# Kernel tuning notes

Measured on AMD Instinct MI355X. Metric: run time of the kernel, lower is better.

Reference implementation:

```python
import jax, jax.numpy as jnp
import numpy as np

B, C, H, W = 4, 512, 64, 64
MID = C // 8  # 64


def setup_inputs() -> dict:
    key = jax.random.key(0)
    ks = jax.random.split(key, 8)
    s = 0.02
    return {
        "x": jax.random.normal(ks[0], (B, C, H, W), dtype=jnp.float32),
        "Wq": jax.random.normal(ks[1], (MID, C), dtype=jnp.float32) * s,
        "bq": jax.random.normal(ks[2], (MID,), dtype=jnp.float32) * s,
        "Wk": jax.random.normal(ks[3], (MID, C), dtype=jnp.float32) * s,
        "bk": jax.random.normal(ks[4], (MID,), dtype=jnp.float32) * s,
        "Wv": jax.random.normal(ks[5], (C, C), dtype=jnp.float32) * s,
        "bv": jax.random.normal(ks[6], (C,), dtype=jnp.float32) * s,
        "gamma": jax.random.uniform(ks[7], (1,), dtype=jnp.float32),
    }


def reference(x, Wq, bq, Wk, bk, Wv, bv, gamma):
    b, c, h, w = x.shape
    n = h * w
    xf = x.reshape(b, c, n)  # [B, C, N]
    # 1x1 convs are per-position linear maps
    q = jnp.einsum('mc,bcn->bnm', Wq, xf) + bq            # [B, N, mid]
    k = jnp.einsum('mc,bcn->bmn', Wk, xf) + bk[:, None]   # [B, mid, N]
    sim = jax.nn.softmax(jnp.einsum('bnm,bmj->bnj', q, k), axis=-1)  # [B, N, N]
    v = jnp.einsum('dc,bcn->bdn', Wv, xf) + bv[:, None]   # [B, C, N]
    # feat[:, d, i] = sum_j v[:, d, j] * sim[:, i, j]
    feat = jnp.einsum('bdj,bij->bdi', v, sim)             # [B, C, N]
    out = gamma[0] * feat + xf
    return out.reshape(b, c, h, w)
```

## Files before the change

### kernel.cpp

```cpp
#include <hip/hip_runtime.h>

#define BATCH 4
#define CCH   512
#define NN    4096
#define MIDD  64

typedef unsigned short u16;
typedef unsigned int   u32;
typedef short s8v  __attribute__((ext_vector_type(8)));
typedef float f16v __attribute__((ext_vector_type(16)));

__device__ __forceinline__ u16 f2bf(float f) {
  u32 u = __float_as_uint(f);
  u += 0x7fffu + ((u >> 16) & 1u);
  return (u16)(u >> 16);
}

__device__ __forceinline__ void g2lds16(const u16* g, u16* l) {
  __builtin_amdgcn_global_load_lds(
      (const __attribute__((address_space(1))) u32*)(const void*)g,
      (__attribute__((address_space(3))) u32*)(void*)l, 16, 0, 0);
}

#define S_WAITCNT(vm, lgkm) \
  __builtin_amdgcn_s_waitcnt(((vm) & 15) | (((vm) >> 4) << 14) | (0x7 << 4) | ((lgkm) << 8))

__global__ __launch_bounds__(256) void prep_w(
    const float* __restrict__ Wq, const float* __restrict__ Wk,
    const float* __restrict__ Wv, u16* __restrict__ Wb)
{
  int e = (blockIdx.x * 256 + threadIdx.x) * 8;
  const float* src;
  if (e < 64 * 512)       src = Wq + e;
  else if (e < 128 * 512) src = Wk + (e - 64 * 512);
  else                    src = Wv + (e - 128 * 512);
  float4 v0 = *(const float4*)src;
  float4 v1 = *(const float4*)(src + 4);
  uint4 p;
  p.x = (u32)f2bf(v0.x) | ((u32)f2bf(v0.y) << 16);
  p.y = (u32)f2bf(v0.z) | ((u32)f2bf(v0.w) << 16);
  p.z = (u32)f2bf(v1.x) | ((u32)f2bf(v1.y) << 16);
  p.w = (u32)f2bf(v1.z) | ((u32)f2bf(v1.w) << 16);
  *(uint4*)(Wb + e) = p;
}

__global__ __launch_bounds__(256) void transpose_cast(
    const float* __restrict__ x, u16* __restrict__ xbT)
{
  const int b  = blockIdx.z;
  const int c0 = blockIdx.y * 64;
  const int n0 = blockIdx.x * 64;
  const int t  = threadIdx.x;
  __shared__ float ts[64 * 65];

  #pragma unroll
  for (int k = 0; k < 4; k++) {
    int idx = t + 256 * k;
    int cc = idx >> 4, n4 = idx & 15;
    float4 v = *(const float4*)&x[((size_t)(b * CCH + c0 + cc)) * NN + n0 + n4 * 4];
    float* p = &ts[cc * 65 + n4 * 4];
    p[0] = v.x; p[1] = v.y; p[2] = v.z; p[3] = v.w;
  }
  __syncthreads();

  const int n = t >> 2, cb = (t & 3) * 16;
  u16 tmp[16];
  #pragma unroll
  for (int j = 0; j < 16; j++) tmp[j] = f2bf(ts[(cb + j) * 65 + n]);
  u16* dst = &xbT[((size_t)b * NN + n0 + n) * CCH + c0 + cb];
  *(uint4*)&dst[0] = *(uint4*)&tmp[0];
  *(uint4*)&dst[8] = *(uint4*)&tmp[8];
}

__global__ __launch_bounds__(256, 2) void proj_gemm(
    const u16* __restrict__ xbT, const u16* __restrict__ Wb,
    const float* __restrict__ bq, const float* __restrict__ bk,
    const float* __restrict__ bv,
    u16* __restrict__ qT, u16* __restrict__ kT, u16* __restrict__ vT)
{
  const int b  = blockIdx.z;
  const int mt = blockIdx.y;
  const int n0 = blockIdx.x * 256;
  const int t  = threadIdx.x;
  const int ln = t & 31, hi = (t & 63) >> 5, w = t >> 6;
  const int l  = t & 63;
  const int l2 = l & 3, lr = l >> 2;
  const int swc = (l2 ^ (lr & 3)) * 8;

  const int mrow0 = (mt < 8) ? (128 + mt * 64) : ((mt == 8) ? 0 : 64);
  const float* bias = (mt < 8) ? (bv + mt * 64) : ((mt == 8) ? bq : bk);

  __shared__ u16 ws[2][64 * 32];
  __shared__ u16 xs[2][256 * 32];

  const u16* xsrc = xbT + ((size_t)b * NN + n0 + w * 64 + lr) * CCH + swc;
  const u16* wsrc = Wb + (size_t)(mrow0 + w * 16 + lr) * 512 + swc;

  f16v acc[4];
  #pragma unroll
  for (int i = 0; i < 4; i++)
    #pragma unroll
    for (int r = 0; r < 16; r++) acc[i][r] = 0.f;

  #pragma unroll
  for (int i = 0; i < 4; i++)
    g2lds16(xsrc + (size_t)(16 * i) * CCH, &xs[0][(w * 64 + i * 16) * 32]);
  g2lds16(wsrc, &ws[0][w * 16 * 32]);

  for (int it = 0; it < 16; it++) {
    const int cur = it & 1, nxt = cur ^ 1;
    __builtin_amdgcn_s_barrier();
    const int c1 = ((it + 1) & 15) * 32;
    #pragma unroll
    for (int i = 0; i < 4; i++)
      g2lds16(xsrc + (size_t)(16 * i) * CCH + c1, &xs[nxt][(w * 64 + i * 16) * 32]);
    g2lds16(wsrc + c1, &ws[nxt][w * 16 * 32]);

    S_WAITCNT(5, 15);
    __builtin_amdgcn_s_barrier();

    #pragma unroll
    for (int ks = 0; ks < 2; ks++) {
      const int cb = ((2 * ks + hi) ^ (ln & 3)) << 3;
      s8v a0 = *(const s8v*)&ws[cur][(ln)           * 32 + cb];
      s8v a1 = *(const s8v*)&ws[cur][(32 + ln)      * 32 + cb];
      s8v b0 = *(const s8v*)&xs[cur][(w * 64 + ln)      * 32 + cb];
      s8v b1 = *(const s8v*)&xs[cur][(w * 64 + 32 + ln) * 32 + cb];
      acc[0] = __builtin_amdgcn_mfma_f32_32x32x16_bf16(a0, b0, acc[0], 0, 0, 0);
      acc[1] = __builtin_amdgcn_mfma_f32_32x32x16_bf16(a0, b1, acc[1], 0, 0, 0);
      acc[2] = __builtin_amdgcn_mfma_f32_32x32x16_bf16(a1, b0, acc[2], 0, 0, 0);
      acc[3] = __builtin_amdgcn_mfma_f32_32x32x16_bf16(a1, b1, acc[3], 0, 0, 0);
    }
  }

  S_WAITCNT(0, 0);
  __builtin_amdgcn_s_barrier();

  if (mt < 8) {
    const int m0g = mt * 64;
    #pragma unroll
    for (int mi = 0; mi < 2; mi++)
      #pragma unroll
      for (int ni = 0; ni < 2; ni++) {
        f16v& a = acc[mi * 2 + ni];
        #pragma unroll
        for (int r = 0; r < 16; r++) {
          int row = (r & 3) + 8 * (r >> 2) + 4 * hi;
          int m   = mi * 32 + row;
          float val = a[r] + bias[m];
          vT[((size_t)b * CCH + m0g + m) * NN + n0 + w * 64 + ni * 32 + ln] = f2bf(val);
        }
      }
  } else {
    u16* dst = (mt == 8) ? qT : kT;
    u16* xt  = &xs[0][0];
    #pragma unroll
    for (int mi = 0; mi < 2; mi++)
      #pragma unroll
      for (int ni = 0; ni < 2; ni++) {
        f16v& a = acc[mi * 2 + ni];
        #pragma unroll
        for (int r = 0; r < 16; r++) {
          int row = (r & 3) + 8 * (r >> 2) + 4 * hi;
          int m   = mi * 32 + row;
          int nr  = w * 64 + ni * 32 + ln;
          xt[(nr << 6) + (((m >> 3) ^ (ln & 7)) << 3) + (m & 7)] = f2bf(a[r] + bias[m]);
        }
      }
    __syncthreads();
    const int r7 = t & 7;
    u16* drow = &dst[((size_t)b * NN + n0 + t) * 64];
    #pragma unroll
    for (int k = 0; k < 8; k++)
      *(uint4*)&drow[k * 8] = *(uint4*)&xt[(t << 6) + ((k ^ r7) << 3)];
  }
}

__global__ __launch_bounds__(256, 2) void attn_kernel(
    const u16* __restrict__ qT,
    const u16* __restrict__ kT,
    const u16* __restrict__ vT,
    const float* __restrict__ x,
    const float* __restrict__ gamma,
    float* __restrict__ out)
{
  __shared__ u16 ksm[2][64 * 64];
  __shared__ u16 plm[2][64 * 64];
  __shared__ u16 vsm[256 * 64];

  const int bx    = blockIdx.x;
  const int slot  = bx & 7;
  const int b     = slot >> 1;
  const int dbase = (slot & 1) * 256;
  const int i0    = (bx >> 3) * 64;
  const int t     = threadIdx.x;
  const int l     = t & 63, ln = l & 31, hi = l >> 5;
  const int w     = t >> 6;
  const int qh    = w >> 1;
  const int jh    = w & 1;
  const int l3    = l & 7, lh3 = l >> 3;
  const int sw8   = (l3 ^ lh3) * 8;

  s8v qfrag[4];
  {
    const u16* qp = qT + ((size_t)b * NN + i0 + qh * 32 + ln) * 64 + hi * 8;
    #pragma unroll
    for (int k = 0; k < 4; k++) qfrag[k] = *(const s8v*)(qp + 16 * k);
  }

  const u16* kbase = kT + (size_t)b * NN * 64;
  const u16* vbase = vT + ((size_t)b * CCH + dbase) * NN;
  const u16* ksrc  = kbase + (size_t)(16 * w + lh3) * 64 + sw8;
  const u16* vsrc  = vbase + (size_t)(64 * w + lh3) * NN + sw8;

  f16v oacc[4];
  #pragma unroll
  for (int i = 0; i < 4; i++)
    #pragma unroll
    for (int r = 0; r < 16; r++) oacc[i][r] = 0.f;
  float lpart[16];
  #pragma unroll
  for (int r = 0; r < 16; r++) lpart[r] = 0.f;

  #pragma unroll
  for (int i = 0; i < 2; i++)
    g2lds16(ksrc + (size_t)(8 * i) * 64, &ksm[0][(w * 2 + i) * 512]);

  for (int it = 0; it < 64; it++) {
    const int j0  = it * 64;
    const int cur = it & 1, nxt = cur ^ 1;

    __builtin_amdgcn_s_barrier();
    #pragma unroll
    for (int i = 0; i < 8; i++)
      g2lds16(vsrc + (size_t)(8 * i) * NN + j0, vsm + (w * 8 + i) * 512);
    const int j1 = ((it + 1) & 63) * 64;
    #pragma unroll
    for (int i = 0; i < 2; i++)
      g2lds16(ksrc + (size_t)(j1 + 8 * i) * 64, &ksm[nxt][(w * 2 + i) * 512]);

    S_WAITCNT(10, 15);
    __builtin_amdgcn_s_barrier();

    f16v sacc;
    #pragma unroll
    for (int r = 0; r < 16; r++) sacc[r] = 0.f;
    #pragma unroll
    for (int ks = 0; ks < 4; ks++) {
      s8v bf = *(const s8v*)&ksm[cur][(jh * 32 + ln) * 64 + (((2 * ks + hi) ^ l3) << 3)];
      sacc = __builtin_amdgcn_mfma_f32_32x32x16_bf16(qfrag[ks], bf, sacc, 0, 0, 0);
    }
    #pragma unroll
    for (int r = 0; r < 16; r++) {
      float p = __expf(sacc[r]);
      lpart[r] += p;
      int row = qh * 32 + (r & 3) + ((r >> 2) << 3) + (hi << 2);
      int r7  = (r & 3) + (hi << 2);
      int jbl = (jh << 2) + (ln >> 3);
      plm[cur][(row << 6) + ((jbl ^ r7) << 3) + (ln & 7)] = f2bf(p);
    }

    S_WAITCNT(2, 0);
    __builtin_amdgcn_s_barrier();

    #pragma unroll
    for (int ks = 0; ks < 4; ks++) {
      const int cb = ((2 * ks + hi) ^ l3) << 3;
      s8v p0 = *(const s8v*)&plm[cur][(ln << 6) + cb];
      s8v p1 = *(const s8v*)&plm[cur][((32 + ln) << 6) + cb];
      s8v v0 = *(const s8v*)&vsm[(((w << 5) + ln) << 6) + cb];
      s8v v1 = *(const s8v*)&vsm[((((w + 4) << 5) + ln) << 6) + cb];
      oacc[0] = __builtin_amdgcn_mfma_f32_32x32x16_bf16(v0, p0, oacc[0], 0, 0, 0);
      oacc[1] = __builtin_amdgcn_mfma_f32_32x32x16_bf16(v0, p1, oacc[1], 0, 0, 0);
      oacc[2] = __builtin_amdgcn_mfma_f32_32x32x16_bf16(v1, p0, oacc[2], 0, 0, 0);
      oacc[3] = __builtin_amdgcn_mfma_f32_32x32x16_bf16(v1, p1, oacc[3], 0, 0, 0);
    }
  }

  S_WAITCNT(0, 0);
  __builtin_amdgcn_s_barrier();

  float* lred = (float*)&ksm[0][0];
  #pragma unroll
  for (int r = 0; r < 16; r++) {
    float v = lpart[r];
    v += __shfl_xor(v, 1);  v += __shfl_xor(v, 2);  v += __shfl_xor(v, 4);
    v += __shfl_xor(v, 8);  v += __shfl_xor(v, 16);
    lpart[r] = v;
  }
  if (ln == 0) {
    #pragma unroll
    for (int r = 0; r < 16; r++) {
      int row = qh * 32 + (r & 3) + ((r >> 2) << 3) + (hi << 2);
      lred[jh * 64 + row] = lpart[r];
    }
  }
  __syncthreads();

  const float g0 = gamma[0];
  #pragma unroll
  for (int qt = 0; qt < 2; qt++) {
    const float linv = 1.0f / (lred[qt * 32 + ln] + lred[64 + qt * 32 + ln]);
    const int n = i0 + qt * 32 + ln;
    #pragma unroll
    for (int ds = 0; ds < 2; ds++) {
      f16v& a = oacc[ds * 2 + qt];
      const int dg = dbase + (w + 4 * ds) * 32;
      #pragma unroll
      for (int r = 0; r < 16; r++) {
        int dl = (r & 3) + 8 * (r >> 2) + 4 * hi;
        size_t idx = ((size_t)b * CCH + dg + dl) * NN + n;
        out[idx] = g0 * a[r] * linv + x[idx];
      }
    }
  }
}

extern "C" void kernel_launch(void* const* d_in, const int* in_sizes, int n_in,
                              void* d_out, int out_size, void* d_ws, size_t ws_size,
                              hipStream_t stream) {
  const float* x     = (const float*)d_in[0];
  const float* Wq    = (const float*)d_in[1];
  const float* bq    = (const float*)d_in[2];
  const float* Wk    = (const float*)d_in[3];
  const float* bk    = (const float*)d_in[4];
  const float* Wv    = (const float*)d_in[5];
  const float* bv    = (const float*)d_in[6];
  const float* gamma = (const float*)d_in[7];
  float* out = (float*)d_out;

  u16* qT  = (u16*)d_ws;
  u16* kT  = qT  + (size_t)BATCH * NN * MIDD;
  u16* vT  = kT  + (size_t)BATCH * NN * MIDD;
  u16* xbT = vT  + (size_t)BATCH * CCH * NN;
  u16* Wb  = xbT + (size_t)BATCH * NN * CCH;

  prep_w<<<dim3(160), 256, 0, stream>>>(Wq, Wk, Wv, Wb);
  transpose_cast<<<dim3(NN / 64, CCH / 64, BATCH), 256, 0, stream>>>(x, xbT);
  proj_gemm<<<dim3(NN / 256, 10, BATCH), 256, 0, stream>>>(
      xbT, Wb, bq, bk, bv, qT, kT, vT);
  attn_kernel<<<dim3(512), 256, 0, stream>>>(qT, kT, vT, x, gamma, out);
}
```

Before: 234.1 us.

## Fuse x transpose/cast into projection GEMM and retile to 128x128 blocks

Removes the separate transpose_cast kernel and its bf16 transposed copy of x. The projection GEMM now loads fp32 x tiles directly into LDS, converts and transposes them in shared memory, and computes 128-row output groups, with q and k merged into one group. Biases are packed into a single buffer by prep_w. This saves a full write and read of a 16 MB intermediate and one launch, but the GEMM loop loses its double buffering, adds extra barriers, and re-reads x five times in fp32.

```diff
diff --git a/kernel.cpp b/kernel.cpp
--- a/kernel.cpp
+++ b/kernel.cpp
@@ -16,10 +16,10 @@
   return (u16)(u >> 16);
 }
 
-__device__ __forceinline__ void g2lds16(const u16* g, u16* l) {
+__device__ __forceinline__ void g2lds16(const void* g, void* l) {
   __builtin_amdgcn_global_load_lds(
-      (const __attribute__((address_space(1))) u32*)(const void*)g,
-      (__attribute__((address_space(3))) u32*)(void*)l, 16, 0, 0);
+      (const __attribute__((address_space(1))) u32*)g,
+      (__attribute__((address_space(3))) u32*)l, 16, 0, 0);
 }
 
 #define S_WAITCNT(vm, lgkm) \
@@ -27,74 +27,53 @@
 
 __global__ __launch_bounds__(256) void prep_w(
     const float* __restrict__ Wq, const float* __restrict__ Wk,
-    const float* __restrict__ Wv, u16* __restrict__ Wb)
-{
-  int e = (blockIdx.x * 256 + threadIdx.x) * 8;
-  const float* src;
-  if (e < 64 * 512)       src = Wq + e;
-  else if (e < 128 * 512) src = Wk + (e - 64 * 512);
-  else                    src = Wv + (e - 128 * 512);
-  float4 v0 = *(const float4*)src;
-  float4 v1 = *(const float4*)(src + 4);
-  uint4 p;
-  p.x = (u32)f2bf(v0.x) | ((u32)f2bf(v0.y) << 16);
-  p.y = (u32)f2bf(v0.z) | ((u32)f2bf(v0.w) << 16);
-  p.z = (u32)f2bf(v1.x) | ((u32)f2bf(v1.y) << 16);
-  p.w = (u32)f2bf(v1.z) | ((u32)f2bf(v1.w) << 16);
-  *(uint4*)(Wb + e) = p;
-}
-
-__global__ __launch_bounds__(256) void transpose_cast(
-    const float* __restrict__ x, u16* __restrict__ xbT)
-{
-  const int b  = blockIdx.z;
-  const int c0 = blockIdx.y * 64;
-  const int n0 = blockIdx.x * 64;
-  const int t  = threadIdx.x;
-  __shared__ float ts[64 * 65];
-
-  #pragma unroll
-  for (int k = 0; k < 4; k++) {
-    int idx = t + 256 * k;
-    int cc = idx >> 4, n4 = idx & 15;
-    float4 v = *(const float4*)&x[((size_t)(b * CCH + c0 + cc)) * NN + n0 + n4 * 4];
-    float* p = &ts[cc * 65 + n4 * 4];
-    p[0] = v.x; p[1] = v.y; p[2] = v.z; p[3] = v.w;
-  }
-  __syncthreads();
-
-  const int n = t >> 2, cb = (t & 3) * 16;
-  u16 tmp[16];
-  #pragma unroll
-  for (int j = 0; j < 16; j++) tmp[j] = f2bf(ts[(cb + j) * 65 + n]);
-  u16* dst = &xbT[((size_t)b * NN + n0 + n) * CCH + c0 + cb];
-  *(uint4*)&dst[0] = *(uint4*)&tmp[0];
-  *(uint4*)&dst[8] = *(uint4*)&tmp[8];
-}
-
-__global__ __launch_bounds__(256, 2) void proj_gemm(
-    const u16* __restrict__ xbT, const u16* __restrict__ Wb,
+    const float* __restrict__ Wv,
     const float* __restrict__ bq, const float* __restrict__ bk,
     const float* __restrict__ bv,
+    u16* __restrict__ Wb, float* __restrict__ bb)
+{
+  const int bid = blockIdx.x;
+  const int t   = threadIdx.x;
+  if (bid < 160) {
+    int e = (bid * 256 + t) * 8;
+    const float* src;
+    if (e < 64 * 512)       src = Wq + e;
+    else if (e < 128 * 512) src = Wk + (e - 64 * 512);
+    else                    src = Wv + (e - 128 * 512);
+    float4 v0 = *(const float4*)src;
+    float4 v1 = *(const float4*)(src + 4);
+    uint4 p;
+    p.x = (u32)f2bf(v0.x) | ((u32)f2bf(v0.y) << 16);
+    p.y = (u32)f2bf(v0.z) | ((u32)f2bf(v0.w) << 16);
+    p.z = (u32)f2bf(v1.x) | ((u32)f2bf(v1.y) << 16);
+    p.w = (u32)f2bf(v1.z) | ((u32)f2bf(v1.w) << 16);
+    *(uint4*)(Wb + e) = p;
+  } else if (t < 160) {
+    int e = t * 4;
+    const float* s = (t < 16) ? (bq + e) : (t < 32) ? (bk + (e - 64)) : (bv + (e - 128));
+    *(float4*)&bb[e] = *(const float4*)s;
+  }
+}
+
+__global__ __launch_bounds__(256, 2) void proj_gemm(
+    const float* __restrict__ x, const u16* __restrict__ Wb,
+    const float* __restrict__ bb,
     u16* __restrict__ qT, u16* __restrict__ kT, u16* __restrict__ vT)
 {
-  const int b  = blockIdx.z;
-  const int mt = blockIdx.y;
-  const int n0 = blockIdx.x * 256;
+  __shared__ char smem[32768];
+  float* xf  = (float*)smem;
+  u16*   xb  = (u16*)(smem + 16384);
+  u16*   wsm = (u16*)(smem + 24576);
+
+  const int b     = blockIdx.z;
+  const int g     = blockIdx.y;
+  const int gn0   = blockIdx.x * 128;
+  const int mrow0 = g * 128;
   const int t  = threadIdx.x;
-  const int ln = t & 31, hi = (t & 63) >> 5, w = t >> 6;
-  const int l  = t & 63;
-  const int l2 = l & 3, lr = l >> 2;
-  const int swc = (l2 ^ (lr & 3)) * 8;
-
-  const int mrow0 = (mt < 8) ? (128 + mt * 64) : ((mt == 8) ? 0 : 64);
-  const float* bias = (mt < 8) ? (bv + mt * 64) : ((mt == 8) ? bq : bk);
-
-  __shared__ u16 ws[2][64 * 32];
-  __shared__ u16 xs[2][256 * 32];
-
-  const u16* xsrc = xbT + ((size_t)b * NN + n0 + w * 64 + lr) * CCH + swc;
-  const u16* wsrc = Wb + (size_t)(mrow0 + w * 16 + lr) * 512 + swc;
+  const int l  = t & 63, ln = l & 31, hi = l >> 5, w = t >> 6;
+
+  const float* xsrc = x + ((size_t)(b * CCH) + w * 8 + (l >> 5)) * NN + gn0 + (l & 31) * 4;
+  const u16* wsrc = Wb + (size_t)(mrow0 + w * 32 + (l >> 2)) * 512 + ((l & 3) ^ ((l >> 2) & 3)) * 8;
 
   f16v acc[4];
   #pragma unroll
@@ -102,77 +81,78 @@
     #pragma unroll
     for (int r = 0; r < 16; r++) acc[i][r] = 0.f;
 
-  #pragma unroll
-  for (int i = 0; i < 4; i++)
-    g2lds16(xsrc + (size_t)(16 * i) * CCH, &xs[0][(w * 64 + i * 16) * 32]);
-  g2lds16(wsrc, &ws[0][w * 16 * 32]);
+  const int nrow = t >> 1, ch = (t & 1) * 16;
 
   for (int it = 0; it < 16; it++) {
-    const int cur = it & 1, nxt = cur ^ 1;
-    __builtin_amdgcn_s_barrier();
-    const int c1 = ((it + 1) & 15) * 32;
+    const int c0 = it * 32;
+    __syncthreads();
     #pragma unroll
     for (int i = 0; i < 4; i++)
-      g2lds16(xsrc + (size_t)(16 * i) * CCH + c1, &xs[nxt][(w * 64 + i * 16) * 32]);
-    g2lds16(wsrc + c1, &ws[nxt][w * 16 * 32]);
-
-    S_WAITCNT(5, 15);
-    __builtin_amdgcn_s_barrier();
+      g2lds16(xsrc + (size_t)(c0 + 2 * i) * NN, xf + (w * 8 + 2 * i) * 128);
+    #pragma unroll
+    for (int i = 0; i < 2; i++)
+      g2lds16(wsrc + (size_t)(i * 16) * 512 + c0, wsm + (w * 32 + i * 16) * 32);
+    __syncthreads();
+
+    u32 pk[8];
+    #pragma unroll
+    for (int j2 = 0; j2 < 8; j2++) {
+      float f0 = xf[(ch + 2 * j2 + 0) * 128 + nrow];
+      float f1 = xf[(ch + 2 * j2 + 1) * 128 + nrow];
+      pk[j2] = (u32)f2bf(f0) | ((u32)f2bf(f1) << 16);
+    }
+    #pragma unroll
+    for (int p2 = 0; p2 < 2; p2++) {
+      int phys = ((ch >> 3) + p2) ^ (nrow & 3);
+      *(uint4*)&xb[(nrow << 5) + (phys << 3)] =
+          make_uint4(pk[p2 * 4], pk[p2 * 4 + 1], pk[p2 * 4 + 2], pk[p2 * 4 + 3]);
+    }
+    __syncthreads();
 
     #pragma unroll
     for (int ks = 0; ks < 2; ks++) {
       const int cb = ((2 * ks + hi) ^ (ln & 3)) << 3;
-      s8v a0 = *(const s8v*)&ws[cur][(ln)           * 32 + cb];
-      s8v a1 = *(const s8v*)&ws[cur][(32 + ln)      * 32 + cb];
-      s8v b0 = *(const s8v*)&xs[cur][(w * 64 + ln)      * 32 + cb];
-      s8v b1 = *(const s8v*)&xs[cur][(w * 64 + 32 + ln) * 32 + cb];
-      acc[0] = __builtin_amdgcn_mfma_f32_32x32x16_bf16(a0, b0, acc[0], 0, 0, 0);
-      acc[1] = __builtin_amdgcn_mfma_f32_32x32x16_bf16(a0, b1, acc[1], 0, 0, 0);
-      acc[2] = __builtin_amdgcn_mfma_f32_32x32x16_bf16(a1, b0, acc[2], 0, 0, 0);
-      acc[3] = __builtin_amdgcn_mfma_f32_32x32x16_bf16(a1, b1, acc[3], 0, 0, 0);
-    }
-  }
-
-  S_WAITCNT(0, 0);
-  __builtin_amdgcn_s_barrier();
-
-  if (mt < 8) {
-    const int m0g = mt * 64;
-    #pragma unroll
-    for (int mi = 0; mi < 2; mi++)
+      s8v bf = *(const s8v*)&xb[((w * 32 + ln) << 5) + cb];
       #pragma unroll
-      for (int ni = 0; ni < 2; ni++) {
-        f16v& a = acc[mi * 2 + ni];
-        #pragma unroll
-        for (int r = 0; r < 16; r++) {
-          int row = (r & 3) + 8 * (r >> 2) + 4 * hi;
-          int m   = mi * 32 + row;
-          float val = a[r] + bias[m];
-          vT[((size_t)b * CCH + m0g + m) * NN + n0 + w * 64 + ni * 32 + ln] = f2bf(val);
-        }
+      for (int ms = 0; ms < 4; ms++) {
+        s8v af = *(const s8v*)&wsm[((ms * 32 + ln) << 5) + cb];
+        acc[ms] = __builtin_amdgcn_mfma_f32_32x32x16_bf16(af, bf, acc[ms], 0, 0, 0);
+      }
+    }
+  }
+  __syncthreads();
+
+  if (g > 0) {
+    const int d0 = mrow0 - 128;
+    #pragma unroll
+    for (int ms = 0; ms < 4; ms++)
+      #pragma unroll
+      for (int r = 0; r < 16; r++) {
+        int m = ms * 32 + (r & 3) + 8 * (r >> 2) + 4 * hi;
+        float val = acc[ms][r] + bb[mrow0 + m];
+        vT[((size_t)b * CCH + d0 + m) * NN + gn0 + w * 32 + ln] = f2bf(val);
       }
   } else {
-    u16* dst = (mt == 8) ? qT : kT;
-    u16* xt  = &xs[0][0];
-    #pragma unroll
-    for (int mi = 0; mi < 2; mi++)
+    u16* scr = (u16*)smem;
+    const int n = w * 32 + ln;
+    #pragma unroll
+    for (int ms = 0; ms < 4; ms++)
       #pragma unroll
-      for (int ni = 0; ni < 2; ni++) {
-        f16v& a = acc[mi * 2 + ni];
-        #pragma unroll
-        for (int r = 0; r < 16; r++) {
-          int row = (r & 3) + 8 * (r >> 2) + 4 * hi;
-          int m   = mi * 32 + row;
-          int nr  = w * 64 + ni * 32 + ln;
-          xt[(nr << 6) + (((m >> 3) ^ (ln & 7)) << 3) + (m & 7)] = f2bf(a[r] + bias[m]);
-        }
+      for (int r2 = 0; r2 < 8; r2++) {
+        int r = 2 * r2;
+        int m = ms * 32 + (r & 3) + 8 * (r >> 2) + 4 * hi;
+        u32 p = (u32)f2bf(acc[ms][r] + bb[m]) |
+                ((u32)f2bf(acc[ms][r + 1] + bb[m + 1]) << 16);
+        *(u32*)&scr[(n << 7) + ((((m >> 3) ^ (n & 15))) << 3) + (m & 7)] = p;
       }
     __syncthreads();
-    const int r7 = t & 7;
-    u16* drow = &dst[((size_t)b * NN + n0 + t) * 64];
-    #pragma unroll
-    for (int k = 0; k < 8; k++)
-      *(uint4*)&drow[k * 8] = *(uint4*)&xt[(t << 6) + ((k ^ r7) << 3)];
+    const int nr = t >> 1, half = t & 1;
+    u16* drow = (half ? kT : qT) + ((size_t)b * NN + gn0 + nr) * 64;
+    #pragma unroll
+    for (int k = 0; k < 8; k++) {
+      int phys = (half * 8 + k) ^ (nr & 15);
+      *(uint4*)&drow[k * 8] = *(const uint4*)&scr[(nr << 7) + (phys << 3)];
+    }
   }
 }
 
@@ -329,15 +309,13 @@
   const float* gamma = (const float*)d_in[7];
   float* out = (float*)d_out;
 
-  u16* qT  = (u16*)d_ws;
-  u16* kT  = qT  + (size_t)BATCH * NN * MIDD;
-  u16* vT  = kT  + (size_t)BATCH * NN * MIDD;
-  u16* xbT = vT  + (size_t)BATCH * CCH * NN;
-  u16* Wb  = xbT + (size_t)BATCH * NN * CCH;
-
-  prep_w<<<dim3(160), 256, 0, stream>>>(Wq, Wk, Wv, Wb);
-  transpose_cast<<<dim3(NN / 64, CCH / 64, BATCH), 256, 0, stream>>>(x, xbT);
-  proj_gemm<<<dim3(NN / 256, 10, BATCH), 256, 0, stream>>>(
-      xbT, Wb, bq, bk, bv, qT, kT, vT);
+  u16*   qT = (u16*)d_ws;
+  u16*   kT = qT + (size_t)BATCH * NN * MIDD;
+  u16*   vT = kT + (size_t)BATCH * NN * MIDD;
+  u16*   Wb = vT + (size_t)BATCH * CCH * NN;
+  float* bb = (float*)(Wb + (size_t)640 * 512);
+
+  prep_w<<<dim3(161), 256, 0, stream>>>(Wq, Wk, Wv, bq, bk, bv, Wb, bb);
+  proj_gemm<<<dim3(NN / 128, 5, BATCH), 256, 0, stream>>>(x, Wb, bb, qT, kT, vT);
   attn_kernel<<<dim3(512), 256, 0, stream>>>(qT, kT, vT, x, gamma, out);
 }
```

New measurement: 237.6 us. No clear change (+1.5%).
